# Kernel tuning notes

Measured on AMD Instinct MI355X. Metric: run time of the kernel, lower is better.

The kernel has to match this reference:

```python
import jax, jax.numpy as jnp
import numpy as np

N, E, D, L = 50000, 600000, 128, 2  # nodes, edges, hidden_dim, num_gnn_layers
NEG_SLOPE = 0.2  # PyG GATv2Conv default negative_slope


def setup_inputs() -> dict:
    key = jax.random.key(0)
    ks = jax.random.split(key, 10)
    s = 1.0 / np.sqrt(D)
    return {
        "x": jax.random.normal(ks[0], (N, D), jnp.float32),
        "edge_index": jax.random.randint(ks[1], (2, E), 0, N, dtype=jnp.int32),
        # per-layer GATv2 params (stacked over L layers)
        "Wl": jax.random.normal(ks[2], (L, D, D), jnp.float32) * s,  # lin_l (source)
        "bl": jnp.zeros((L, D), jnp.float32),
        "Wr": jax.random.normal(ks[3], (L, D, D), jnp.float32) * s,  # lin_r (target)
        "br": jnp.zeros((L, D), jnp.float32),
        "att": jax.random.normal(ks[4], (L, D), jnp.float32) * s,
        "bias": jnp.zeros((L, D), jnp.float32),
        # shared residual Linear
        "W_res": jax.random.normal(ks[5], (D, D), jnp.float32) * s,
        "b_res": jnp.zeros((D,), jnp.float32),
    }


def reference(x, edge_index, Wl, bl, Wr, br, att, bias, W_res, b_res):
    n = x.shape[0]
    # add self loops (PyG GATv2Conv default add_self_loops=True)
    loops = jnp.arange(n, dtype=edge_index.dtype)
    src = jnp.concatenate([edge_index[0], loops])  # source j (messages)
    dst = jnp.concatenate([edge_index[1], loops])  # target i (aggregation)

    def conv(h, i):
        xl = h @ Wl[i] + bl[i]  # [N, D] source transform
        xr = h @ Wr[i] + br[i]  # [N, D] target transform
        m = xl[src] + xr[dst]   # [E+N, D] gathered edge messages
        e = jnp.einsum('ed,d->e', jnp.where(m > 0, m, NEG_SLOPE * m), att[i])
        # segment softmax over incoming edges of each destination node
        emax = jax.lax.stop_gradient(jax.ops.segment_max(e, dst, num_segments=n))
        ex = jnp.exp(e - emax[dst])
        denom = jax.ops.segment_sum(ex, dst, num_segments=n)
        alpha = ex / (denom[dst] + 1e-16)
        out = jax.ops.segment_sum(alpha[:, None] * xl[src], dst, num_segments=n)
        return out + bias[i]

    for i in range(Wl.shape[0]):
        x = jax.nn.relu(conv(x, i) + x @ W_res + b_res)
    return x
```

## Files before the change

### kernel.cpp

```cpp
#include <hip/hip_runtime.h>
#include <math.h>


#define DIM 128
#define NEG_SLOPE 0.2f
#define TPW 4

typedef __attribute__((ext_vector_type(8))) short short8;
typedef __attribute__((ext_vector_type(4))) float floatx4;
typedef __attribute__((ext_vector_type(2))) float f32x2;

static __device__ __forceinline__ unsigned short f2b(float f) {
    unsigned u = __float_as_uint(f);
    unsigned r = (u + 0x7FFFu + ((u >> 16) & 1u)) >> 16;
    return (unsigned short)r;
}
static __device__ __forceinline__ f32x2 cvt2(unsigned u) {
    f32x2 r;
    r.x = __uint_as_float(u << 16);
    r.y = __uint_as_float(u & 0xffff0000u);
    return r;
}
static __device__ __forceinline__ f32x2 pk_add(f32x2 a, f32x2 b) {
    f32x2 d;
    asm("v_pk_add_f32 %0, %1, %2" : "=v"(d) : "v"(a), "v"(b));
    return d;
}
static __device__ __forceinline__ f32x2 pk_mul(f32x2 a, f32x2 b) {
    f32x2 d;
    asm("v_pk_mul_f32 %0, %1, %2" : "=v"(d) : "v"(a), "v"(b));
    return d;
}
static __device__ __forceinline__ f32x2 pk_fma(f32x2 a, f32x2 b, f32x2 c) {
    f32x2 d;
    asm("v_pk_fma_f32 %0, %1, %2, %3" : "=v"(d) : "v"(a), "v"(b), "v"(c));
    return d;
}
static __device__ __forceinline__ f32x2 absf2(f32x2 a) {
    f32x2 r;
    r.x = __builtin_fabsf(a.x);
    r.y = __builtin_fabsf(a.y);
    return r;
}

__global__ void k_count(const int* __restrict__ dst, int E, int* __restrict__ counts) {
    int k = blockIdx.x * blockDim.x + threadIdx.x;
    if (k < E) atomicAdd(&counts[dst[k]], 1);
}

__global__ void k_scan1(const int* __restrict__ counts, int n,
                        int* __restrict__ rowptr, int* __restrict__ bsum) {
    __shared__ int s[256];
    int tid = threadIdx.x;
    int i = blockIdx.x * 256 + tid;
    int v = (i < n) ? (counts[i] + 1) : 0;
    s[tid] = v;
    __syncthreads();
    for (int off = 1; off < 256; off <<= 1) {
        int t = (tid >= off) ? s[tid - off] : 0;
        __syncthreads();
        s[tid] += t;
        __syncthreads();
    }
    if (i < n) rowptr[i + 1] = s[tid];
    if (tid == 255) bsum[blockIdx.x] = s[255];
}

__global__ void k_scan2(int* __restrict__ bsum, int nb) {
    __shared__ int s[256];
    int tid = threadIdx.x;
    int v = (tid < nb) ? bsum[tid] : 0;
    s[tid] = v;
    __syncthreads();
    for (int off = 1; off < 256; off <<= 1) {
        int t = (tid >= off) ? s[tid - off] : 0;
        __syncthreads();
        s[tid] += t;
        __syncthreads();
    }
    if (tid < nb) bsum[tid] = s[tid];
}

__global__ void k_scan3(int* __restrict__ rowptr, const int* __restrict__ bsum,
                        int n, int* __restrict__ counts_to_cursors) {
    int i = blockIdx.x * 256 + threadIdx.x;
    if (i < n) {
        int add = (blockIdx.x > 0) ? bsum[blockIdx.x - 1] : 0;
        int cnt = counts_to_cursors[i] + 1;
        int v = rowptr[i + 1] + add;
        rowptr[i + 1] = v;
        counts_to_cursors[i] = v - cnt;
    }
    if (i == 0) rowptr[0] = 0;
}

__global__ void k_scatter(const int* __restrict__ src, const int* __restrict__ dst,
                          int E, int n, int* __restrict__ cur, int* __restrict__ srt) {
    int k = blockIdx.x * blockDim.x + threadIdx.x;
    int tot = E + n;
    if (k >= tot) return;
    int s, d;
    if (k < E) { s = src[k]; d = dst[k]; }
    else       { s = k - E;  d = s; }
    int p = atomicAdd(&cur[d], 1);
    srt[p] = s;
}

__global__ void k_pre(const float* __restrict__ Wl, const float* __restrict__ Wr,
                      const float* __restrict__ Wres, unsigned short* __restrict__ wfrag,
                      const float* __restrict__ h, unsigned short* __restrict__ hfrag,
                      int n, int ntiles) {
    int blk = blockIdx.x;
    if (blk < 48) {
        int idx = blk * 256 + threadIdx.x;
        int lane = idx & 63;
        int nr   = (idx >> 6) & 7;
        int ks   = (idx >> 9) & 3;
        int v    = idx >> 11;
        int sec = v % 3, l = v / 3;
        const float* W = (sec == 0) ? (Wl + l * DIM * DIM)
                       : (sec == 1) ? (Wr + l * DIM * DIM) : Wres;
        int nn = nr * 16 + (lane & 15);
        int k0 = ks * 32 + ((lane >> 4) << 3);
        ushort4 a, b;
        a.x = f2b(W[(k0 + 0) * DIM + nn]); a.y = f2b(W[(k0 + 1) * DIM + nn]);
        a.z = f2b(W[(k0 + 2) * DIM + nn]); a.w = f2b(W[(k0 + 3) * DIM + nn]);
        b.x = f2b(W[(k0 + 4) * DIM + nn]); b.y = f2b(W[(k0 + 5) * DIM + nn]);
        b.z = f2b(W[(k0 + 6) * DIM + nn]); b.w = f2b(W[(k0 + 7) * DIM + nn]);
        *(ushort4*)(wfrag + (size_t)idx * 8) = a;
        *(ushort4*)(wfrag + (size_t)idx * 8 + 4) = b;
    } else {
        int idx = (blk - 48) * 256 + threadIdx.x;
        if (idx >= ntiles * 256) return;
        int lane = idx & 63;
        int ks   = (idx >> 6) & 3;
        int tile = idx >> 8;
        int row  = tile * 16 + (lane & 15);
        int col0 = ks * 32 + ((lane >> 4) << 3);
        ushort4 a = {0, 0, 0, 0}, b = {0, 0, 0, 0};
        if (row < n) {
            float4 v0 = *(const float4*)(h + (size_t)row * DIM + col0);
            float4 v1 = *(const float4*)(h + (size_t)row * DIM + col0 + 4);
            a.x = f2b(v0.x); a.y = f2b(v0.y); a.z = f2b(v0.z); a.w = f2b(v0.w);
            b.x = f2b(v1.x); b.y = f2b(v1.y); b.z = f2b(v1.z); b.w = f2b(v1.w);
        }
        *(ushort4*)(hfrag + (size_t)idx * 8) = a;
        *(ushort4*)(hfrag + (size_t)idx * 8 + 4) = b;
    }
}

__global__ __launch_bounds__(256, 2) void k_gemm(
    const unsigned short* __restrict__ hfrag, const unsigned short* __restrict__ wfrag,
    const float* __restrict__ bl, const float* __restrict__ br, const float* __restrict__ bres,
    unsigned short* __restrict__ XLb, unsigned short* __restrict__ XRb,
    float* __restrict__ RES, int ntiles)
{
    int sec  = blockIdx.y;
    int lane = threadIdx.x & 63;
    int w    = threadIdx.x >> 6;

    const unsigned short* wbase = wfrag + (size_t)sec * (4 * 8 * 64 * 8);
    short8 bf[4][8];
#pragma unroll
    for (int ks = 0; ks < 4; ks++)
#pragma unroll
        for (int nr = 0; nr < 8; nr++)
            bf[ks][nr] = *(const short8*)(wbase + (((ks * 8 + nr) * 64 + lane) << 3));

    const float* bias = (sec == 0) ? bl : (sec == 1) ? br : bres;
    int colb = (lane >> 4) << 2;
    float4 bv[8];
#pragma unroll
    for (int nr = 0; nr < 8; nr++) bv[nr] = *(const float4*)(bias + nr * 16 + colb);

    int wid = blockIdx.x * 4 + w;
#pragma unroll
    for (int i = 0; i < TPW; i++) {
        int t = wid * TPW + i;
        if (t >= ntiles) break;
        short8 a[4];
#pragma unroll
        for (int ks = 0; ks < 4; ks++)
            a[ks] = *(const short8*)(hfrag + (((t * 4 + ks) * 64 + lane) << 3));
        floatx4 acc[8];
#pragma unroll
        for (int nr = 0; nr < 8; nr++) acc[nr] = (floatx4){0.f, 0.f, 0.f, 0.f};
#pragma unroll
        for (int ks = 0; ks < 4; ks++)
#pragma unroll
            for (int nr = 0; nr < 8; nr++)
                acc[nr] = __builtin_amdgcn_mfma_f32_16x16x32_bf16(bf[ks][nr], a[ks], acc[nr], 0, 0, 0);

        int row = t * 16 + (lane & 15);
        size_t rb = (size_t)row * DIM;
#pragma unroll
        for (int nr = 0; nr < 8; nr++) {
            float4 o;
            o.x = acc[nr][0] + bv[nr].x;
            o.y = acc[nr][1] + bv[nr].y;
            o.z = acc[nr][2] + bv[nr].z;
            o.w = acc[nr][3] + bv[nr].w;
            int col = nr * 16 + colb;
            if (sec == 2) {
                *(float4*)(RES + rb + col) = o;
            } else {
                ushort4 u;
                u.x = f2b(o.x); u.y = f2b(o.y); u.z = f2b(o.z); u.w = f2b(o.w);
                if (sec == 0) *(ushort4*)(XLb + rb + col) = u;
                else          *(ushort4*)(XRb + rb + col) = u;
            }
        }
    }
}

#define EDGE_P(K)                                                        \
    f32x2 v01_##K = cvt2(e##K.x), v23_##K = cvt2(e##K.y);                \
    float p##K;                                                          \
    {                                                                    \
        f32x2 t01 = pk_add(v01_##K, x01);                                \
        f32x2 t23 = pk_add(v23_##K, x23);                                \
        f32x2 pp = pk_mul(a6_01, t01);                                   \
        pp = pk_fma(a4_01, absf2(t01), pp);                              \
        pp = pk_fma(a6_23, t23, pp);                                     \
        pp = pk_fma(a4_23, absf2(t23), pp);                              \
        p##K = pp.x + pp.y;                                              \
    }

__global__ __launch_bounds__(256) void k_aggr(
    const unsigned short* __restrict__ XLb, const unsigned short* __restrict__ XRb,
    const float* __restrict__ RES, const float* __restrict__ att,
    const float* __restrict__ bias, const int* __restrict__ rowptr,
    const int* __restrict__ srt, float* __restrict__ outF,
    unsigned short* __restrict__ fragOut, int writeFrag, int n)
{
    int wave = threadIdx.x >> 6;
    int lane = threadIdx.x & 63;
    int node = blockIdx.x * 4 + wave;
    if (node >= n) return;
    int half = lane >> 5, sl = lane & 31;
    int d0 = sl << 2;

    float4 af = *(const float4*)(att + d0);
    f32x2 a6_01 = {0.6f * af.x, 0.6f * af.y}, a6_23 = {0.6f * af.z, 0.6f * af.w};
    f32x2 a4_01 = {0.4f * af.x, 0.4f * af.y}, a4_23 = {0.4f * af.z, 0.4f * af.w};

    uint2 xru = *(const uint2*)(XRb + (size_t)node * DIM + d0);
    f32x2 x01 = cvt2(xru.x), x23 = cvt2(xru.y);

    int beg = rowptr[node], end = rowptr[node + 1];
    int len = end - beg;
    int hl = (len + 1) >> 1;
    int sb = beg + half * hl;
    int se = half ? end : (beg + hl);

    const uint2* R = (const uint2*)XLb;

    f32x2 acc01 = {0.f, 0.f}, acc23 = {0.f, 0.f};
    float den = 0.f;

    for (int j = sb; j < se; j += 4) {
        int j1 = (j + 1 < se) ? j + 1 : j;
        int j2 = (j + 2 < se) ? j + 2 : j;
        int j3 = (j + 3 < se) ? j + 3 : j;
        int s0 = srt[j], s1 = srt[j1], s2 = srt[j2], s3 = srt[j3];
        uint2 e0 = R[(size_t)s0 * 32 + sl];
        uint2 e1 = R[(size_t)s1 * 32 + sl];
        uint2 e2 = R[(size_t)s2 * 32 + sl];
        uint2 e3 = R[(size_t)s3 * 32 + sl];
        EDGE_P(0) EDGE_P(1) EDGE_P(2) EDGE_P(3)
#pragma unroll
        for (int off = 16; off >= 1; off >>= 1) {
            p0 += __shfl_xor(p0, off);
            p1 += __shfl_xor(p1, off);
            p2 += __shfl_xor(p2, off);
            p3 += __shfl_xor(p3, off);
        }
        float w0 = __expf(fminf(p0, 80.f));
        float w1 = (j + 1 < se) ? __expf(fminf(p1, 80.f)) : 0.f;
        float w2 = (j + 2 < se) ? __expf(fminf(p2, 80.f)) : 0.f;
        float w3 = (j + 3 < se) ? __expf(fminf(p3, 80.f)) : 0.f;
        den += (w0 + w1) + (w2 + w3);
        acc01 = pk_fma((f32x2){w0, w0}, v01_0, acc01);
        acc23 = pk_fma((f32x2){w0, w0}, v23_0, acc23);
        acc01 = pk_fma((f32x2){w1, w1}, v01_1, acc01);
        acc23 = pk_fma((f32x2){w1, w1}, v23_1, acc23);
        acc01 = pk_fma((f32x2){w2, w2}, v01_2, acc01);
        acc23 = pk_fma((f32x2){w2, w2}, v23_2, acc23);
        acc01 = pk_fma((f32x2){w3, w3}, v01_3, acc01);
        acc23 = pk_fma((f32x2){w3, w3}, v23_3, acc23);
    }

    den     += __shfl_xor(den, 32);
    acc01.x += __shfl_xor(acc01.x, 32);
    acc01.y += __shfl_xor(acc01.y, 32);
    acc23.x += __shfl_xor(acc23.x, 32);
    acc23.y += __shfl_xor(acc23.y, 32);
    if (half) return;

    float inv = 1.f / (den + 1e-16f);
    float4 r4 = *(const float4*)(RES + (size_t)node * DIM + d0);
    float4 b4 = *(const float4*)(bias + d0);
    float4 o;
    o.x = fmaxf(acc01.x * inv + b4.x + r4.x, 0.f);
    o.y = fmaxf(acc01.y * inv + b4.y + r4.y, 0.f);
    o.z = fmaxf(acc23.x * inv + b4.z + r4.z, 0.f);
    o.w = fmaxf(acc23.y * inv + b4.w + r4.w, 0.f);

    if (writeFrag) {
        int tile = node >> 4;
        int ks = sl >> 3;
        int li = (node & 15) + (((sl >> 1) & 3) << 4);
        int j0 = (sl & 1) << 2;
        ushort4 u;
        u.x = f2b(o.x); u.y = f2b(o.y); u.z = f2b(o.z); u.w = f2b(o.w);
        *(ushort4*)(fragOut + ((size_t)((tile * 4 + ks) * 64 + li) << 3) + j0) = u;
    } else {
        *(float4*)(outF + (size_t)node * DIM + d0) = o;
    }
}

extern "C" void kernel_launch(void* const* d_in, const int* in_sizes, int n_in,
                              void* d_out, int out_size, void* d_ws, size_t ws_size,
                              hipStream_t stream) {
    const float* x    = (const float*)d_in[0];
    const int*   ei   = (const int*)d_in[1];
    const float* Wl   = (const float*)d_in[2];
    const float* bl   = (const float*)d_in[3];
    const float* Wr   = (const float*)d_in[4];
    const float* br   = (const float*)d_in[5];
    const float* att  = (const float*)d_in[6];
    const float* bias = (const float*)d_in[7];
    const float* Wres = (const float*)d_in[8];
    const float* bres = (const float*)d_in[9];

    int n = in_sizes[0] / DIM;
    int E = in_sizes[1] / 2;
    int ntiles = (n + 15) >> 4;
    const int* srcIdx = ei;
    const int* dstIdx = ei + E;

    float* resb = (float*)d_ws;
    unsigned short* xlb   = (unsigned short*)(resb + (size_t)n * DIM);
    unsigned short* xrb   = xlb + (size_t)n * DIM;
    unsigned short* hfrag = xrb + (size_t)n * DIM;
    unsigned short* wfrag = hfrag + (size_t)ntiles * 16 * DIM;
    int* rowptr = (int*)(wfrag + 2 * 3 * DIM * DIM);
    int* tmpc   = rowptr + (n + 1);
    int* srt    = tmpc + n;
    int* bsum   = srt + (E + n + 8);

    int nb1 = (n + 255) / 256;

    k_pre<<<48 + ntiles, 256, 0, stream>>>(Wl, Wr, Wres, wfrag, x, hfrag, n, ntiles);
    hipMemsetAsync(tmpc, 0, (size_t)n * sizeof(int), stream);
    k_count<<<(E + 255) / 256, 256, 0, stream>>>(dstIdx, E, tmpc);
    k_scan1<<<nb1, 256, 0, stream>>>(tmpc, n, rowptr, bsum);
    k_scan2<<<1, 256, 0, stream>>>(bsum, nb1);
    k_scan3<<<nb1, 256, 0, stream>>>(rowptr, bsum, n, tmpc);
    k_scatter<<<(E + n + 255) / 256, 256, 0, stream>>>(srcIdx, dstIdx, E, n, tmpc, srt);

    int gx = (ntiles + 4 * TPW - 1) / (4 * TPW);
    for (int l = 0; l < 2; l++) {
        dim3 g(gx, 3);
        k_gemm<<<g, 256, 0, stream>>>(hfrag, wfrag + (size_t)l * 3 * 4 * 8 * 64 * 8,
                                      bl + (size_t)l * DIM, br + (size_t)l * DIM, bres,
                                      xlb, xrb, resb, ntiles);
        k_aggr<<<(n + 3) / 4, 256, 0, stream>>>(xlb, xrb, resb, att + (size_t)l * DIM,
                                                bias + (size_t)l * DIM, rowptr, srt,
                                                (float*)d_out, hfrag, (l == 0) ? 1 : 0, n);
    }
}
```

Measured before the change: 223.3 us.

## Fold memset and scan2 into other kernels, use exp2 with prescaled attention

Zeroes the count array inside the preprocessing kernel instead of a separate memset. Merges the block-sum scan into the final scan kernel, so each block redundantly rescans the block sums. Folds log2(e) into the attention coefficients so exp2 replaces expf, and swaps the inline packed-math asm for plain vector arithmetic left to the compiler. Also sets an occupancy hint of 8 blocks on the aggregation kernel, which may cap its register use.

```diff
diff --git a/kernel.cpp b/kernel.cpp
--- a/kernel.cpp
+++ b/kernel.cpp
@@ -21,22 +21,7 @@
     r.y = __uint_as_float(u & 0xffff0000u);
     return r;
 }
-static __device__ __forceinline__ f32x2 pk_add(f32x2 a, f32x2 b) {
-    f32x2 d;
-    asm("v_pk_add_f32 %0, %1, %2" : "=v"(d) : "v"(a), "v"(b));
-    return d;
-}
-static __device__ __forceinline__ f32x2 pk_mul(f32x2 a, f32x2 b) {
-    f32x2 d;
-    asm("v_pk_mul_f32 %0, %1, %2" : "=v"(d) : "v"(a), "v"(b));
-    return d;
-}
-static __device__ __forceinline__ f32x2 pk_fma(f32x2 a, f32x2 b, f32x2 c) {
-    f32x2 d;
-    asm("v_pk_fma_f32 %0, %1, %2, %3" : "=v"(d) : "v"(a), "v"(b), "v"(c));
-    return d;
-}
-static __device__ __forceinline__ f32x2 absf2(f32x2 a) {
+static __device__ __forceinline__ f32x2 abs2(f32x2 a) {
     f32x2 r;
     r.x = __builtin_fabsf(a.x);
     r.y = __builtin_fabsf(a.y);
@@ -66,7 +51,8 @@
     if (tid == 255) bsum[blockIdx.x] = s[255];
 }
 
-__global__ void k_scan2(int* __restrict__ bsum, int nb) {
+__global__ void k_scan3(int* __restrict__ rowptr, const int* __restrict__ bsum,
+                        int n, int* __restrict__ counts_to_cursors, int nb) {
     __shared__ int s[256];
     int tid = threadIdx.x;
     int v = (tid < nb) ? bsum[tid] : 0;
@@ -78,18 +64,13 @@
         s[tid] += t;
         __syncthreads();
     }
-    if (tid < nb) bsum[tid] = s[tid];
-}
-
-__global__ void k_scan3(int* __restrict__ rowptr, const int* __restrict__ bsum,
-                        int n, int* __restrict__ counts_to_cursors) {
-    int i = blockIdx.x * 256 + threadIdx.x;
+    int add = (blockIdx.x > 0) ? s[blockIdx.x - 1] : 0;
+    int i = blockIdx.x * 256 + tid;
     if (i < n) {
-        int add = (blockIdx.x > 0) ? bsum[blockIdx.x - 1] : 0;
         int cnt = counts_to_cursors[i] + 1;
-        int v = rowptr[i + 1] + add;
-        rowptr[i + 1] = v;
-        counts_to_cursors[i] = v - cnt;
+        int vv = rowptr[i + 1] + add;
+        rowptr[i + 1] = vv;
+        counts_to_cursors[i] = vv - cnt;
     }
     if (i == 0) rowptr[0] = 0;
 }
@@ -109,7 +90,7 @@
 __global__ void k_pre(const float* __restrict__ Wl, const float* __restrict__ Wr,
                       const float* __restrict__ Wres, unsigned short* __restrict__ wfrag,
                       const float* __restrict__ h, unsigned short* __restrict__ hfrag,
-                      int n, int ntiles) {
+                      int* __restrict__ tmpc, int n, int ntiles) {
     int blk = blockIdx.x;
     if (blk < 48) {
         int idx = blk * 256 + threadIdx.x;
@@ -129,9 +110,8 @@
         b.z = f2b(W[(k0 + 6) * DIM + nn]); b.w = f2b(W[(k0 + 7) * DIM + nn]);
         *(ushort4*)(wfrag + (size_t)idx * 8) = a;
         *(ushort4*)(wfrag + (size_t)idx * 8 + 4) = b;
-    } else {
+    } else if (blk < 48 + ntiles) {
         int idx = (blk - 48) * 256 + threadIdx.x;
-        if (idx >= ntiles * 256) return;
         int lane = idx & 63;
         int ks   = (idx >> 6) & 3;
         int tile = idx >> 8;
@@ -146,6 +126,9 @@
         }
         *(ushort4*)(hfrag + (size_t)idx * 8) = a;
         *(ushort4*)(hfrag + (size_t)idx * 8 + 4) = b;
+    } else {
+        int i = (blk - 48 - ntiles) * 256 + threadIdx.x;
+        if (i < n) tmpc[i] = 0;
     }
 }
 
@@ -217,16 +200,15 @@
     f32x2 v01_##K = cvt2(e##K.x), v23_##K = cvt2(e##K.y);                \
     float p##K;                                                          \
     {                                                                    \
-        f32x2 t01 = pk_add(v01_##K, x01);                                \
-        f32x2 t23 = pk_add(v23_##K, x23);                                \
-        f32x2 pp = pk_mul(a6_01, t01);                                   \
-        pp = pk_fma(a4_01, absf2(t01), pp);                              \
-        pp = pk_fma(a6_23, t23, pp);                                     \
-        pp = pk_fma(a4_23, absf2(t23), pp);                              \
+        f32x2 t01 = v01_##K + x01;                                       \
+        f32x2 t23 = v23_##K + x23;                                       \
+        f32x2 pp = a6_01 * t01 + a4_01 * abs2(t01);                      \
+        pp += a6_23 * t23;                                               \
+        pp += a4_23 * abs2(t23);                                         \
         p##K = pp.x + pp.y;                                              \
     }
 
-__global__ __launch_bounds__(256) void k_aggr(
+__global__ __launch_bounds__(256, 8) void k_aggr(
     const unsigned short* __restrict__ XLb, const unsigned short* __restrict__ XRb,
     const float* __restrict__ RES, const float* __restrict__ att,
     const float* __restrict__ bias, const int* __restrict__ rowptr,
@@ -240,9 +222,11 @@
     int half = lane >> 5, sl = lane & 31;
     int d0 = sl << 2;
 
+    const float S6 = 0.6f * 1.44269504089f;
+    const float S4 = 0.4f * 1.44269504089f;
     float4 af = *(const float4*)(att + d0);
-    f32x2 a6_01 = {0.6f * af.x, 0.6f * af.y}, a6_23 = {0.6f * af.z, 0.6f * af.w};
-    f32x2 a4_01 = {0.4f * af.x, 0.4f * af.y}, a4_23 = {0.4f * af.z, 0.4f * af.w};
+    f32x2 a6_01 = {S6 * af.x, S6 * af.y}, a6_23 = {S6 * af.z, S6 * af.w};
+    f32x2 a4_01 = {S4 * af.x, S4 * af.y}, a4_23 = {S4 * af.z, S4 * af.w};
 
     uint2 xru = *(const uint2*)(XRb + (size_t)node * DIM + d0);
     f32x2 x01 = cvt2(xru.x), x23 = cvt2(xru.y);
@@ -275,19 +259,15 @@
             p2 += __shfl_xor(p2, off);
             p3 += __shfl_xor(p3, off);
         }
-        float w0 = __expf(fminf(p0, 80.f));
-        float w1 = (j + 1 < se) ? __expf(fminf(p1, 80.f)) : 0.f;
-        float w2 = (j + 2 < se) ? __expf(fminf(p2, 80.f)) : 0.f;
-        float w3 = (j + 3 < se) ? __expf(fminf(p3, 80.f)) : 0.f;
+        float w0 = __builtin_exp2f(fminf(p0, 120.f));
+        float w1 = (j + 1 < se) ? __builtin_exp2f(fminf(p1, 120.f)) : 0.f;
+        float w2 = (j + 2 < se) ? __builtin_exp2f(fminf(p2, 120.f)) : 0.f;
+        float w3 = (j + 3 < se) ? __builtin_exp2f(fminf(p3, 120.f)) : 0.f;
         den += (w0 + w1) + (w2 + w3);
-        acc01 = pk_fma((f32x2){w0, w0}, v01_0, acc01);
-        acc23 = pk_fma((f32x2){w0, w0}, v23_0, acc23);
-        acc01 = pk_fma((f32x2){w1, w1}, v01_1, acc01);
-        acc23 = pk_fma((f32x2){w1, w1}, v23_1, acc23);
-        acc01 = pk_fma((f32x2){w2, w2}, v01_2, acc01);
-        acc23 = pk_fma((f32x2){w2, w2}, v23_2, acc23);
-        acc01 = pk_fma((f32x2){w3, w3}, v01_3, acc01);
-        acc23 = pk_fma((f32x2){w3, w3}, v23_3, acc23);
+        acc01 += w0 * v01_0 + w1 * v01_1;
+        acc23 += w0 * v23_0 + w1 * v23_1;
+        acc01 += w2 * v01_2 + w3 * v01_3;
+        acc23 += w2 * v23_2 + w3 * v23_3;
     }
 
     den     += __shfl_xor(den, 32);
@@ -351,12 +331,11 @@
 
     int nb1 = (n + 255) / 256;
 
-    k_pre<<<48 + ntiles, 256, 0, stream>>>(Wl, Wr, Wres, wfrag, x, hfrag, n, ntiles);
-    hipMemsetAsync(tmpc, 0, (size_t)n * sizeof(int), stream);
+    k_pre<<<48 + ntiles + nb1, 256, 0, stream>>>(Wl, Wr, Wres, wfrag, x, hfrag,
+                                                 tmpc, n, ntiles);
     k_count<<<(E + 255) / 256, 256, 0, stream>>>(dstIdx, E, tmpc);
     k_scan1<<<nb1, 256, 0, stream>>>(tmpc, n, rowptr, bsum);
-    k_scan2<<<1, 256, 0, stream>>>(bsum, nb1);
-    k_scan3<<<nb1, 256, 0, stream>>>(rowptr, bsum, n, tmpc);
+    k_scan3<<<nb1, 256, 0, stream>>>(rowptr, bsum, n, tmpc, nb1);
     k_scatter<<<(E + n + 255) / 256, 256, 0, stream>>>(srcIdx, dstIdx, E, n, tmpc, srt);
 
     int gx = (ntiles + 4 * TPW - 1) / (4 * TPW);
```

Result: faster. 216.6 us (-3.0%).
